# Optimization experiments

Hardware: AMD Instinct MI355X
Metric: run time of the kernel (lower is better)

The kernel has to match this reference:

```python
import jax, jax.numpy as jnp
import numpy as np

H = 2048; HQ = 16; HKV = 4; G = HQ // HKV; D = 128; S = 2048
KS = 32; KSTRIDE = 16; BS = 128; TOPK = 8
INIT_BLK = 1; LOCAL_BLK = 2; WIN = 512
THETA = 500000.0
N_CMP = (S - KS) // KSTRIDE + 1
N_BLK = S // BS
NEG = -1e30


def _rope_inv_freq():
    # llama3-style frequency scaling (factor 8, high 4, low 1, orig 8192)
    inv = 1.0 / (THETA ** (np.arange(0, D, 2, dtype=np.float64) / D))
    factor, lo_f, hi_f, orig = 8.0, 1.0, 4.0, 8192.0
    wav = 2.0 * np.pi / inv
    smooth = (orig / wav - lo_f) / (hi_f - lo_f)
    inv_s = np.where(wav > orig / lo_f, inv / factor,
                     np.where(wav < orig / hi_f, inv,
                              (1.0 - smooth) * inv / factor + smooth * inv))
    return jnp.asarray(inv_s, dtype=jnp.float32)


def _rope(x):
    # x: [S, h, D]
    ang = jnp.arange(x.shape[0], dtype=jnp.float32)[:, None] * _rope_inv_freq()[None, :]
    cos = jnp.cos(ang)[:, None, :]
    sin = jnp.sin(ang)[:, None, :]
    x1, x2 = x[..., : D // 2], x[..., D // 2:]
    return jnp.concatenate([x1 * cos - x2 * sin, x2 * cos + x1 * sin], axis=-1)


def setup_inputs() -> dict:
    key = jax.random.key(0)
    ks = jax.random.split(key, 8)
    std = 0.02
    return {
        'hidden_states': jax.random.normal(ks[0], (1, S, H), jnp.float32),
        'Wq': jax.random.normal(ks[1], (H, HQ * D), jnp.float32) * std,
        'Wk': jax.random.normal(ks[2], (H, HKV * D), jnp.float32) * std,
        'Wv': jax.random.normal(ks[3], (H, HKV * D), jnp.float32) * std,
        'Wo': jax.random.normal(ks[4], (HQ * D, H), jnp.float32) * std,
        'Wg': jax.random.normal(ks[5], (H, HQ * 3), jnp.float32) * std,
        'Wck': jax.random.normal(ks[6], (HKV, KS * D, D), jnp.float32) * std,
        'Wcv': jax.random.normal(ks[7], (HKV, KS * D, D), jnp.float32) * std,
    }


def _nsa_forward(hidden_states, Wq, Wk, Wv, Wo, Wg, Wck, Wcv):
    x = hidden_states[0]                                  # [S, H] (bsz=1, packed)
    q = _rope((x @ Wq).reshape(S, HQ, D))                 # [S, HQ, D]
    k = _rope((x @ Wk).reshape(S, HKV, D))                # [S, HKV, D]
    v = (x @ Wv).reshape(S, HKV, D)
    scale = D ** -0.5
    pos = jnp.arange(S)
    qg = q.reshape(S, HKV, G, D)

    # ---- branch 1: compressed attention (overlapping windows, learned pooling) ----
    starts = jnp.arange(N_CMP) * KSTRIDE
    widx = starts[:, None] + jnp.arange(KS)[None, :]      # [N_CMP, KS]
    kw = k[widx].transpose(2, 0, 1, 3).reshape(HKV, N_CMP, KS * D)
    vw = v[widx].transpose(2, 0, 1, 3).reshape(HKV, N_CMP, KS * D)
    ck = jnp.einsum('hnf,hfd->hnd', kw, Wck)              # [HKV, N_CMP, D]
    cv = jnp.einsum('hnf,hfd->hnd', vw, Wcv)
    s_cmp = jnp.einsum('shgd,hnd->hgsn', qg, ck) * scale  # [HKV, G, S, N_CMP]
    m_cmp = (starts + KS)[None, :] <= pos[:, None] + 1    # fully-past compressed blocks
    has_cmp = m_cmp.any(axis=-1).astype(s_cmp.dtype)      # [S]
    p_cmp = jax.nn.softmax(jnp.where(m_cmp[None, None], s_cmp, NEG), axis=-1)
    p_cmp = p_cmp * has_cmp[None, None, :, None]
    o_cmp = jnp.einsum('hgsn,hnd->shgd', p_cmp, cv).reshape(S, HQ, D)

    # ---- branch 2: top-k block-selected attention ----
    cmp2blk = (starts // BS)[:, None] == jnp.arange(N_BLK)[None, :]
    bscore = jnp.einsum('hgsn,nb->hsb', p_cmp, cmp2blk.astype(p_cmp.dtype))  # GQA-group sum
    qblk = pos // BS
    blks = jnp.arange(N_BLK)
    forced = (blks[None, :] < INIT_BLK) | ((blks[None, :] <= qblk[:, None]) & (blks[None, :] > qblk[:, None] - LOCAL_BLK))
    _, top_idx = jax.lax.top_k(bscore + forced[None].astype(bscore.dtype) * 1e9, TOPK)
    sel_blk = jnp.any(top_idx[..., None] == blks, axis=-2)  # [HKV, S, N_BLK]

    causal = pos[None, :] <= pos[:, None]                    # [S, S]
    raw = jnp.einsum('shgd,nhd->hgsn', qg, k) * scale        # [HKV, G, S, S] (shared by branches 2/3)

    m_sel = jnp.repeat(sel_blk, BS, axis=-1) & causal[None]  # [HKV, S, S]
    p_sel = jax.nn.softmax(jnp.where(m_sel[:, None], raw, NEG), axis=-1)
    o_sel = jnp.einsum('hgsn,nhd->shgd', p_sel, v).reshape(S, HQ, D)

    # ---- branch 3: sliding-window attention ----
    m_win = causal & (pos[None, :] > pos[:, None] - WIN)
    p_win = jax.nn.softmax(jnp.where(m_win[None, None], raw, NEG), axis=-1)
    o_win = jnp.einsum('hgsn,nhd->shgd', p_win, v).reshape(S, HQ, D)

    # ---- per-head sigmoid gates mixing the three branches ----
    g = jax.nn.sigmoid(x @ Wg).reshape(S, HQ, 3)
    o = g[..., 0:1] * o_cmp + g[..., 1:2] * o_sel + g[..., 2:3] * o_win
    return (o.reshape(S, HQ * D) @ Wo)[None]                 # [1, S, H]


def reference(hidden_states, Wq, Wk, Wv, Wo, Wg, Wck, Wcv):
    return _nsa_forward(hidden_states, Wq, Wk, Wv, Wo, Wg, Wck, Wcv)
```

## Files before the change

### kernel.cpp

```cpp
#include <hip/hip_runtime.h>
#include <math.h>

#define SS 2048
#define HH 2048
#define HQ 16
#define HKV 4
#define GG 4
#define DD 128
#define KS 32
#define KSTRIDE 16
#define NCMP 127
#define NBLK 16
#define TOPK 8
#define WINSZ 512
#define TQ 16

typedef unsigned short u16;
typedef __bf16 bf16x8 __attribute__((ext_vector_type(8)));
typedef __bf16 bf16x4 __attribute__((ext_vector_type(4)));
typedef float f32x4 __attribute__((ext_vector_type(4)));

__device__ __forceinline__ u16 f2bf(float f) {
    __bf16 b = (__bf16)f;
    return __builtin_bit_cast(u16, b);
// ... 189 lines not shown
            bf16x8 af[4], bf[4];
#pragma unroll
            for (int mi = 0; mi < 4; ++mi) {
                int row = wm * 64 + mi * 16 + lr;
                int g = (kk * 4 + hi) ^ (row & 7);
                af[mi] = *reinterpret_cast<const bf16x8*>(&Asm[row * 64 + g * 8]);
            }
#pragma unroll
            for (int ni = 0; ni < 4; ++ni) {
                int row = wn * 64 + ni * 16 + lr;
                int g = (kk * 4 + hi) ^ (row & 7);
                bf[ni] = *reinterpret_cast<const bf16x8*>(&Bsm[row * 64 + g * 8]);
            }
#pragma unroll
            for (int mi = 0; mi < 4; ++mi)
#pragma unroll
                for (int ni = 0; ni < 4; ++ni)
                    acc[mi][ni] = __builtin_amdgcn_mfma_f32_16x16x32_bf16(af[mi], bf[ni], acc[mi][ni], 0, 0, 0);
        }
    }
#pragma unroll
    for (int mi = 0; mi < 4; ++mi) {
#pragma unroll
        for (int ni = 0; ni < 4; ++ni) {
            int col = bn + wn * 64 + ni * 16 + lr;
            if (col < N) {
#pragma unroll
                for (int r = 0; r < 4; ++r) {
                    int row = bm + wm * 64 + mi * 16 + hi * 4 + r;
                    C[(size_t)row * N + col] = acc[mi][ni][r];
                }
            }
        }
    }
}

__global__ __launch_bounds__(256) void cmp_kv_split(const u16* __restrict__ Ak,
                                                    const u16* __restrict__ Wkt,
                                                    const u16* __restrict__ Av,
                                                    const u16* __restrict__ Wvt,
                                                    float* __restrict__ partials) {
    __shared__ __align__(16) u16 Asm[128 * 64];
    __shared__ __align__(16) u16 Bsm[128 * 64];
    int z = blockIdx.y, split = blockIdx.x;
    int h = z & 3;
    const u16* A  = (z >> 2) ? Av : Ak;
    const u16* Wt = (z >> 2) ? Wvt : Wkt;
    int t = threadIdx.x, lane = t & 63, w = t >> 6;
    int wm = w >> 1, wn = w & 1;
    int lr = lane & 15, hi = lane >> 4;
    const u16* Wh = Wt + (size_t)h * DD * (KS * DD);

    f32x4 acc[4][4] = {};
    int kbase = split * 512;
    for (int it = 0; it < 8; ++it) {
        int k0 = kbase + it * 64;
        if (it) __syncthreads();
        int roff = k0 >> 7;
        int dbase = ((k0 >> 6) & 1) * 64;
#pragma unroll
        for (int i = 0; i < 4; ++i) {
            int cflat = i * 256 + t;
            int m = cflat >> 3;
            int g = cflat & 7;
            int gl = g ^ (m & 7);
            unsigned lofs = (unsigned)((i * 256 + (t & ~63)) * 16);
            int nr = (m < NCMP) ? m : (NCMP - 1);
            gload16(A + ((size_t)(nr * KSTRIDE + roff) * HKV + h) * DD + dbase + gl * 8,
                    (char*)Asm + lofs);
            gload16(Wh + (size_t)m * (KS * DD) + k0 + gl * 8, (char*)Bsm + lofs);
        }
        __syncthreads();
#pragma unroll
        for (int kk = 0; kk < 2; ++kk) {
            bf16x8 af[4], bf[4];
#pragma unroll
            for (int mi = 0; mi < 4; ++mi) {
                int row = wm * 64 + mi * 16 + lr;
                int g = (kk * 4 + hi) ^ (row & 7);
                af[mi] = *reinterpret_cast<const bf16x8*>(&Asm[row * 64 + g * 8]);
            }
#pragma unroll
            for (int ni = 0; ni < 4; ++ni) {
                int row = wn * 64 + ni * 16 + lr;
                int g = (kk * 4 + hi) ^ (row & 7);
                bf[ni] = *reinterpret_cast<const bf16x8*>(&Bsm[row * 64 + g * 8]);
            }
#pragma unroll
            for (int mi = 0; mi < 4; ++mi)
#pragma unroll
                for (int ni = 0; ni < 4; ++ni)
                    acc[mi][ni] = __builtin_amdgcn_mfma_f32_16x16x32_bf16(af[mi], bf[ni], acc[mi][ni], 0, 0, 0);
        }
    }
    float* Cout = partials + ((size_t)(z * 8 + split)) * 128 * 128;
#pragma unroll
    for (int mi = 0; mi < 4; ++mi)
#pragma unroll
        for (int ni = 0; ni < 4; ++ni) {
            int col = wn * 64 + ni * 16 + lr;
#pragma unroll
            for (int r = 0; r < 4; ++r) {
                int row = wm * 64 + mi * 16 + hi * 4 + r;
                Cout[(size_t)row * 128 + col] = acc[mi][ni][r];
            }
        }
}

__global__ void cmp_kv_reduce(const float* __restrict__ partials,
                              u16* __restrict__ ckbf, u16* __restrict__ cvtbf) {
    int row = blockIdx.x, z = blockIdx.y, col = threadIdx.x;
    float s = 0.f;
#pragma unroll
    for (int sp = 0; sp < 8; ++sp)
        s += partials[(((size_t)z * 8 + sp) * 128 + row) * 128 + col];
    if (z < 4) ckbf[((size_t)z * 128 + row) * 128 + col] = f2bf(s);
    else       cvtbf[((size_t)(z - 4) * 128 + col) * 128 + row] = f2bf(s);
}

__global__ __launch_bounds__(256) void cmp_attn_mfma(
    const u16* __restrict__ qbf,
    const u16* __restrict__ ckbf,
    const u16* __restrict__ cvtbf,
    const float* __restrict__ gate,
    float* __restrict__ o_acc,
    unsigned int* __restrict__ sel) {
    __shared__ __align__(16) u16 Cks[128 * 128];
    __shared__ __align__(16) u16 P2[4][16 * 128];
    __shared__ float bs[4][16][16];
    int t = threadIdx.x, lane = t & 63, w = t >> 6;
    int lr = lane & 15, hi = lane >> 4;
    int s0 = blockIdx.x * 16, h = blockIdx.y;
    int hq = h * GG + w;
    int sr = s0 + lr;
    const u16* ckh = ckbf + (size_t)h * 128 * 128;
    const u16* cvh = cvtbf + (size_t)h * 128 * 128;
    bf16x8 qf[4];
#pragma unroll
    for (int ks = 0; ks < 4; ++ks)
        qf[ks] = *reinterpret_cast<const bf16x8*>(
            &qbf[((size_t)sr * HQ + hq) * DD + ks * 32 + hi * 8]);
#pragma unroll
    for (int i = 0; i < 8; ++i) {
        int id = i * 256 + t;
        int key = id >> 4, sub = id & 15;
        gload16(ckh + (size_t)key * 128 + ((sub ^ (key & 7)) * 8),
                (char*)Cks + (id & ~63) * 16);
    }
    __syncthreads();
    f32x4 sacc[8] = {};
#pragma unroll
    for (int ks = 0; ks < 4; ++ks)
#pragma unroll
        for (int mt = 0; mt < 8; ++mt) {
            int row = mt * 16 + lr;
            bf16x8 kf = *reinterpret_cast<const bf16x8*>(
                &Cks[row * 128 + (((ks * 4 + hi) ^ (row & 7)) * 8)]);
            sacc[mt] = __builtin_amdgcn_mfma_f32_16x16x32_bf16(kf, qf[ks], sacc[mt], 0, 0, 0);
        }
    int nv = (sr >= 31) ? ((sr - 31) >> 4) + 1 : 0;
    float e[8][4];
    float mx = -1e30f;
#pragma unroll
    for (int mt = 0; mt < 8; ++mt)
#pragma unroll
        for (int r = 0; r < 4; ++r) {
            int n = mt * 16 + hi * 4 + r;
            float x = (n < nv) ? sacc[mt][r] : -1e30f;
            e[mt][r] = x;
            mx = fmaxf(mx, x);
        }
    mx = fmaxf(mx, __shfl_xor(mx, 16, 64));
    mx = fmaxf(mx, __shfl_xor(mx, 32, 64));
    float l = 0.f;
#pragma unroll
    for (int mt = 0; mt < 8; ++mt)
#pragma unroll
        for (int r = 0; r < 4; ++r) {
            int n = mt * 16 + hi * 4 + r;
            float p = (n < nv) ? __expf(e[mt][r] - mx) : 0.f;
            e[mt][r] = p;
            l += p;
        }
    l += __shfl_xor(l, 16, 64);
    l += __shfl_xor(l, 32, 64);
    float invl = (nv > 0) ? 1.f / l : 0.f;
#pragma unroll
    for (int mt = 0; mt < 8; ++mt)
#pragma unroll
        for (int r = 0; r < 4; ++r) e[mt][r] *= invl;
#pragma unroll
    for (int mt = 0; mt < 8; ++mt) {
        bf16x4 pk;
        pk[0] = (__bf16)e[mt][0]; pk[1] = (__bf16)e[mt][1];
        pk[2] = (__bf16)e[mt][2]; pk[3] = (__bf16)e[mt][3];
        int grp = mt * 2 + (hi >> 1);
        int idx = lr * 128 + ((grp ^ (lr & 7)) * 8) + (hi & 1) * 4;
        *reinterpret_cast<bf16x4*>(&P2[w][idx]) = pk;
    }
#pragma unroll
    for (int mt = 0; mt < 8; ++mt) {
        float s4 = e[mt][0] + e[mt][1] + e[mt][2] + e[mt][3];
        float v = s4 + __shfl_xor(s4, 16, 64);
        if (hi == 0) bs[w][lr][mt * 2] = v;
        else if (hi == 2) bs[w][lr][mt * 2 + 1] = v;
    }
    __syncthreads();
    bf16x8 pa[4];
#pragma unroll
    for (int kslot = 0; kslot < 4; ++kslot)
        pa[kslot] = *reinterpret_cast<const bf16x8*>(
            &P2[w][lr * 128 + (((kslot * 4 + hi) ^ (lr & 7)) * 8)]);
    f32x4 Os[8] = {};
#pragma unroll
    for (int nt = 0; nt < 8; ++nt) {
        int d = nt * 16 + lr;
#pragma unroll
        for (int kslot = 0; kslot < 4; ++kslot) {
            bf16x8 bv = *reinterpret_cast<const bf16x8*>(
                &cvh[(size_t)d * 128 + kslot * 32 + hi * 8]);
            Os[nt] = __builtin_amdgcn_mfma_f32_16x16x32_bf16(pa[kslot], bv, Os[nt], 0, 0, 0);
        }
    }
#pragma unroll
    for (int r = 0; r < 4; ++r) {
        int q = hi * 4 + r;
        int srow = s0 + q;
        float g0 = gate[((size_t)srow * HQ + hq) * 3 + 0];
#pragma unroll
        for (int nt = 0; nt < 8; ++nt) {
            size_t idx = ((size_t)srow * HQ + hq) * DD + nt * 16 + lr;
            o_acc[idx] = g0 * Os[nt][r];
        }
    }
    if (t < 16) {
        int q = t, s = s0 + q;
        int qblk = s >> 7;
#pragma unroll
        for (int b = 0; b < 16; ++b) {
            bool forced = (b == 0) || (b <= qblk && b > qblk - 2);
            bs[0][q][b] = bs[0][q][b] + bs[1][q][b] + bs[2][q][b] + bs[3][q][b]
                          + (forced ? 1e9f : 0.f);
        }
        unsigned int mask = 0;
        for (int it = 0; it < TOPK; ++it) {
            int arg = 0; float best = bs[0][q][0];
            for (int b = 1; b < 16; ++b) {
                float x = bs[0][q][b];
                if (x > best) { best = x; arg = b; }
            }
            mask |= 1u << arg;
            bs[0][q][arg] = -1e38f;
        }
        sel[s * HKV + h] = mask;
    }
}

__global__ __launch_bounds__(256, 3) void sel_win_mfma(
    const u16* __restrict__ qbf,
    const u16* __restrict__ kbf,
    const u16* __restrict__ vtbf,
    const float* __restrict__ gate,
    const unsigned int* __restrict__ sel,
    float* __restrict__ o_acc) {
    __shared__ __align__(16) u16 Ks[64 * 128];
    __shared__ __align__(16) u16 Vs[128 * 64];
    __shared__ __align__(16) u16 P2[4][2][16 * 64];
    __shared__ unsigned int sml[16];
    int t = threadIdx.x, lane = t & 63, w = t >> 6;
    int lr = lane & 15, hi = lane >> 4;
    int s0 = (gridDim.x - 1 - blockIdx.x) * 16;
    int h = blockIdx.y;
    int hq = h * GG + w;
    int sr = s0 + lr;
    if (t < 16) sml[t] = sel[(s0 + t) * HKV + h];
    bf16x8 qf[4];
#pragma unroll
    for (int ks = 0; ks < 4; ++ks)
        qf[ks] = *reinterpret_cast<const bf16x8*>(
            &qbf[((size_t)(s0 + lr) * HQ + hq) * DD + ks * 32 + hi * 8]);
    __syncthreads();
    unsigned mymask = sml[lr];
    unsigned orMask = 0;
#pragma unroll
    for (int i = 0; i < 16; ++i) orMask |= sml[i];
    float m_u = -1e30f, l_s = 0.f, l_w = 0.f;
    f32x4 Os[8] = {}, Ow[8] = {};
    int smax = s0 + 15;
    const u16* vbase = vtbf + (size_t)h * DD * SS;

    for (int kb = 0; kb * 128 <= smax; ++kb) {
        bool needSel = (orMask >> kb) & 1u;
        bool selbit = needSel && ((mymask >> kb) & 1u);
        for (int half = 0; half < 2; ++half) {
            int hst = kb * 128 + half * 64;
            if (hst > smax) break;
            bool hWin = (hst + 63 >= s0 - (WINSZ - 1));
            if (!(needSel || hWin)) continue;
            __syncthreads();
#pragma unroll
            for (int i = 0; i < 4; ++i) {
                int id = i * 256 + t;
                int key = id >> 4, dq = id & 15;
                gload16(kbf + ((size_t)(hst + key) * HKV + h) * DD + ((dq ^ (key & 7)) * 8),
                        (char*)Ks + (id & ~63) * 16);
                int d = id >> 3, kq = id & 7;
                gload16(vbase + (size_t)d * SS + hst + ((kq ^ (d & 7)) * 8),
                        (char*)Vs + (id & ~63) * 16);
            }
            __syncthreads();
            f32x4 sacc[4] = {};
#pragma unroll
            for (int ks = 0; ks < 4; ++ks) {
#pragma unroll
                for (int mt = 0; mt < 4; ++mt) {
                    int key = mt * 16 + lr;
                    bf16x8 kf = *reinterpret_cast<const bf16x8*>(
                        &Ks[key * 128 + (((ks * 4 + hi) ^ (key & 7)) * 8)]);
                    sacc[mt] = __builtin_amdgcn_mfma_f32_16x16x32_bf16(kf, qf[ks], sacc[mt], 0, 0, 0);
                }
            }
            float e4[4][4];
            float mx = -1e30f;
#pragma unroll
            for (int mt = 0; mt < 4; ++mt)
#pragma unroll
                for (int r = 0; r < 4; ++r) {
                    int key = hst + mt * 16 + hi * 4 + r;
                    bool vS = selbit && (key <= sr);
                    bool vW = hWin && (key <= sr) && (key > sr - WINSZ);
                    float e = (vS || vW) ? sacc[mt][r] : -1e30f;
                    e4[mt][r] = e;
                    mx = fmaxf(mx, e);
                }
            mx = fmaxf(mx, __shfl_xor(mx, 16, 64));
            mx = fmaxf(mx, __shfl_xor(mx, 32, 64));
            if (!__all(mx - m_u <= 8.f)) {
                float newm = fmaxf(m_u, mx);
                float corr = __expf(m_u - newm);
                m_u = newm;
                l_s *= corr; l_w *= corr;
#pragma unroll
                for (int r = 0; r < 4; ++r) {
                    float c2 = __shfl(corr, hi * 4 + r, 64);
#pragma unroll
                    for (int nt = 0; nt < 8; ++nt) { Os[nt][r] *= c2; Ow[nt][r] *= c2; }
                }
            }
            float lsA = 0.f, lwA = 0.f;
#pragma unroll
            for (int mt = 0; mt < 4; ++mt)
#pragma unroll
                for (int r = 0; r < 4; ++r) {
                    int key = hst + mt * 16 + hi * 4 + r;
                    bool vS = selbit && (key <= sr);
                    bool vW = hWin && (key <= sr) && (key > sr - WINSZ);
                    float e = (vS || vW) ? __expf(e4[mt][r] - m_u) : 0.f;
                    e4[mt][r] = e;
                    lsA += vS ? e : 0.f;
                    lwA += vW ? e : 0.f;
                }
            lsA += __shfl_xor(lsA, 16, 64); lsA += __shfl_xor(lsA, 32, 64);
            lwA += __shfl_xor(lwA, 16, 64); lwA += __shfl_xor(lwA, 32, 64);
            l_s += lsA; l_w += lwA;
            if (needSel) {
#pragma unroll
                for (int mt = 0; mt < 4; ++mt) {
                    bf16x4 pk;
#pragma unroll
                    for (int r = 0; r < 4; ++r) {
                        int key = hst + mt * 16 + hi * 4 + r;
                        bool vS = selbit && (key <= sr);
                        pk[r] = (__bf16)(vS ? e4[mt][r] : 0.f);
                    }
                    int grp = mt * 2 + (hi >> 1);
                    int idx = lr * 64 + ((grp ^ (lr & 7)) * 8) + (hi & 1) * 4;
                    *reinterpret_cast<bf16x4*>(&P2[w][0][idx]) = pk;
                }
            }
            if (hWin) {
#pragma unroll
                for (int mt = 0; mt < 4; ++mt) {
                    bf16x4 pk;
#pragma unroll
                    for (int r = 0; r < 4; ++r) {
                        int key = hst + mt * 16 + hi * 4 + r;
                        bool vW = (key <= sr) && (key > sr - WINSZ);
                        pk[r] = (__bf16)(vW ? e4[mt][r] : 0.f);
                    }
                    int grp = mt * 2 + (hi >> 1);
                    int idx = lr * 64 + ((grp ^ (lr & 7)) * 8) + (hi & 1) * 4;
                    *reinterpret_cast<bf16x4*>(&P2[w][1][idx]) = pk;
                }
            }
            bf16x8 pas0, pas1, paw0, paw1;
            if (needSel) {
                pas0 = *reinterpret_cast<const bf16x8*>(&P2[w][0][lr * 64 + (((0 + hi) ^ (lr & 7)) * 8)]);
                pas1 = *reinterpret_cast<const bf16x8*>(&P2[w][0][lr * 64 + (((4 + hi) ^ (lr & 7)) * 8)]);
            }
            if (hWin) {
                paw0 = *reinterpret_cast<const bf16x8*>(&P2[w][1][lr * 64 + (((0 + hi) ^ (lr & 7)) * 8)]);
                paw1 = *reinterpret_cast<const bf16x8*>(&P2[w][1][lr * 64 + (((4 + hi) ^ (lr & 7)) * 8)]);
            }
#pragma unroll
            for (int nt = 0; nt < 8; ++nt) {
                int d = nt * 16 + lr;
                bf16x8 bv0 = *reinterpret_cast<const bf16x8*>(&Vs[d * 64 + (((0 + hi) ^ (d & 7)) * 8)]);
                bf16x8 bv1 = *reinterpret_cast<const bf16x8*>(&Vs[d * 64 + (((4 + hi) ^ (d & 7)) * 8)]);
                if (needSel) {
                    Os[nt] = __builtin_amdgcn_mfma_f32_16x16x32_bf16(pas0, bv0, Os[nt], 0, 0, 0);
                    Os[nt] = __builtin_amdgcn_mfma_f32_16x16x32_bf16(pas1, bv1, Os[nt], 0, 0, 0);
                }
                if (hWin) {
                    Ow[nt] = __builtin_amdgcn_mfma_f32_16x16x32_bf16(paw0, bv0, Ow[nt], 0, 0, 0);
                    Ow[nt] = __builtin_amdgcn_mfma_f32_16x16x32_bf16(paw1, bv1, Ow[nt], 0, 0, 0);
                }
            }
        }
    }
    float invls = (l_s > 0.f) ? 1.f / l_s : 0.f;
    float invlw = (l_w > 0.f) ? 1.f / l_w : 0.f;
#pragma unroll
    for (int r = 0; r < 4; ++r) {
        int q = hi * 4 + r;
        int srow = s0 + q;
        float a1 = gate[((size_t)srow * HQ + hq) * 3 + 1] * __shfl(invls, q, 64);
        float a2 = gate[((size_t)srow * HQ + hq) * 3 + 2] * __shfl(invlw, q, 64);
#pragma unroll
        for (int nt = 0; nt < 8; ++nt) {
            size_t idx = ((size_t)srow * HQ + hq) * DD + nt * 16 + lr;
            o_acc[idx] += a1 * Os[nt][r] + a2 * Ow[nt][r];
        }
    }
}

extern "C" void kernel_launch(void* const* d_in, const int* in_sizes, int n_in,
                              void* d_out, int out_size, void* d_ws, size_t ws_size,
                              hipStream_t stream) {
    const float* x   = (const float*)d_in[0];
    const float* Wq  = (const float*)d_in[1];
    const float* Wk  = (const float*)d_in[2];
    const float* Wv  = (const float*)d_in[3];
    const float* Wo  = (const float*)d_in[4];
    const float* Wg  = (const float*)d_in[5];
    const float* Wck = (const float*)d_in[6];
    const float* Wcv = (const float*)d_in[7];
    float* out = (float*)d_out;
    char* w = (char*)d_ws;
    float* qb   = (float*)(w + 0);
    float* kb   = (float*)(w + 16777216);
    float* vb   = (float*)(w + 20971520);
    float* g3   = (float*)(w + 25165824);
    u16* ckbf   = (u16*)(w + 25559040);
    u16* cvtbf  = (u16*)(w + 25819136);
    unsigned int* selb = (unsigned int*)(w + 26079232);
    float* cost = (float*)(w + 26112000);
    float* sint = (float*)(w + 26636288);
    float* oacc = (float*)(w + 27160576);
    u16* xb     = (u16*)(w + 43937792);
    u16* oaccb  = (u16*)(w + 52326400);
    u16* Wq_t   = (u16*)(w + 60715008);
    u16* Wo_t   = (u16*)(w + 69103616);
    u16* Wk_t   = (u16*)(w + 77492224);
    u16* Wv_t   = (u16*)(w + 79589376);
    u16* Wg_t   = (u16*)(w + 81686528);
    u16* qbf = Wq_t;
    u16* kbf = Wk_t;
    u16* vtbf = Wv_t;
    u16* vbf = (u16*)kb;
    u16* Wck_t = oaccb;
    u16* Wcv_t = xb;
    float* partials = oacc;

    hipLaunchKernelGGL(rope_tab, dim3(SS), dim3(64), 0, stream, cost, sint);
    hipLaunchKernelGGL(conv_bf16, dim3(4096), dim3(256), 0, stream, x, xb, SS * HH / 4);
    hipLaunchKernelGGL(convT, dim3(64, 64), dim3(256), 0, stream, Wq, Wq_t, HH, 2048, 2048, 0, 0);
    hipLaunchKernelGGL(convT, dim3(64, 16), dim3(256), 0, stream, Wk, Wk_t, HH, 512, 512, 0, 0);
    hipLaunchKernelGGL(convT, dim3(64, 16), dim3(256), 0, stream, Wv, Wv_t, HH, 512, 512, 0, 0);
    hipLaunchKernelGGL(convT, dim3(64, 4),  dim3(256), 0, stream, Wg, Wg_t, HH, 48, 128, 0, 0);
    hipLaunchKernelGGL(convT, dim3(64, 64), dim3(256), 0, stream, Wo, Wo_t, HQ * DD, 2048, 2048, 0, 0);
    hipLaunchKernelGGL(gemm_proj, dim3(25, 16), dim3(256), 0, stream,
                       xb, Wq_t, Wk_t, Wv_t, Wg_t, qb, kb, vb, g3);
    hipLaunchKernelGGL(rope_bf16, dim3(SS, HQ),  dim3(64), 0, stream, qb, qbf, cost, sint, HQ, 0.08838834764831845f);
    hipLaunchKernelGGL(rope_bf16, dim3(SS, HKV), dim3(64), 0, stream, kb, kbf, cost, sint, HKV, 1.0f);
    hipLaunchKernelGGL(sigmoid_k, dim3((SS * HQ * 3 + 255) / 256), dim3(256), 0, stream, g3, SS * HQ * 3);
    hipLaunchKernelGGL(conv_bf16, dim3(1024), dim3(256), 0, stream, vb, vbf, SS * HKV * DD / 4);
    hipLaunchKernelGGL(conv_vt, dim3(64, 4, 4), dim3(256), 0, stream, vb, vtbf);
    hipLaunchKernelGGL(convT, dim3(128, 4, 4), dim3(256), 0, stream,
                       Wck, Wck_t, KS * DD, DD, DD, (size_t)KS * DD * DD, (size_t)DD * KS * DD);
    hipLaunchKernelGGL(convT, dim3(128, 4, 4), dim3(256), 0, stream,
                       Wcv, Wcv_t, KS * DD, DD, DD, (size_t)KS * DD * DD, (size_t)DD * KS * DD);
    hipLaunchKernelGGL(cmp_kv_split, dim3(8, 8), dim3(256), 0, stream,
                       kbf, Wck_t, vbf, Wcv_t, partials);
    hipLaunchKernelGGL(cmp_kv_reduce, dim3(128, 8), dim3(128), 0, stream,
                       partials, ckbf, cvtbf);
    hipLaunchKernelGGL(cmp_attn_mfma, dim3(SS / TQ, HKV), dim3(256), 0, stream,
                       qbf, ckbf, cvtbf, g3, oacc, selb);
    hipLaunchKernelGGL(sel_win_mfma, dim3(SS / TQ, HKV), dim3(256), 0, stream,
                       qbf, kbf, vtbf, g3, selb, oacc);
    hipLaunchKernelGGL(conv_bf16, dim3(4096), dim3(256), 0, stream, oacc, oaccb, SS * HQ * DD / 4);
    hipLaunchKernelGGL(gemm_mfma, dim3(16, 16), dim3(256), 0, stream, oaccb, Wo_t, out, 2048, 2048, 2048);
}
```

Measured before the change: 266.1 us.

## Fuse compressed and selected/window attention into one kernel; widen cmp-KV split

Merges the compressed-attention kernel and the selection/sliding-window kernel into a single attn_fused kernel. The top-k block mask now passes through shared memory, and the final output is written directly as bf16, which removes the fp32 o_acc round trip, the separate sel buffer and the conv_bf16 launch. Shared memory is reused between the compressed KV tile and the K/V tiles. The cmp_kv_split grid is also doubled to 16 splits with half the K range each, giving more parallelism at the cost of a larger reduction. The fused kernel holds the extra Oc accumulators in registers, which may raise register pressure under launch bounds of 3.

```diff
diff --git a/kernel.cpp b/kernel.cpp
--- a/kernel.cpp
+++ b/kernel.cpp
@@ -265,8 +265,8 @@
     const u16* Wh = Wt + (size_t)h * DD * (KS * DD);
 
     f32x4 acc[4][4] = {};
-    int kbase = split * 512;
-    for (int it = 0; it < 8; ++it) {
+    int kbase = split * 256;
+    for (int it = 0; it < 4; ++it) {
         int k0 = kbase + it * 64;
         if (it) __syncthreads();
         int roff = k0 >> 7;
@@ -306,7 +306,7 @@
                     acc[mi][ni] = __builtin_amdgcn_mfma_f32_16x16x32_bf16(af[mi], bf[ni], acc[mi][ni], 0, 0, 0);
         }
     }
-    float* Cout = partials + ((size_t)(z * 8 + split)) * 128 * 128;
+    float* Cout = partials + ((size_t)(z * 16 + split)) * 128 * 128;
 #pragma unroll
     for (int mi = 0; mi < 4; ++mi)
 #pragma unroll
@@ -325,160 +325,23 @@
     int row = blockIdx.x, z = blockIdx.y, col = threadIdx.x;
     float s = 0.f;
 #pragma unroll
-    for (int sp = 0; sp < 8; ++sp)
-        s += partials[(((size_t)z * 8 + sp) * 128 + row) * 128 + col];
+    for (int sp = 0; sp < 16; ++sp)
+        s += partials[(((size_t)z * 16 + sp) * 128 + row) * 128 + col];
     if (z < 4) ckbf[((size_t)z * 128 + row) * 128 + col] = f2bf(s);
     else       cvtbf[((size_t)(z - 4) * 128 + col) * 128 + row] = f2bf(s);
 }
 
-__global__ __launch_bounds__(256) void cmp_attn_mfma(
+__global__ __launch_bounds__(256, 3) void attn_fused(
     const u16* __restrict__ qbf,
+    const u16* __restrict__ kbf,
+    const u16* __restrict__ vtbf,
     const u16* __restrict__ ckbf,
     const u16* __restrict__ cvtbf,
     const float* __restrict__ gate,
-    float* __restrict__ o_acc,
-    unsigned int* __restrict__ sel) {
-    __shared__ __align__(16) u16 Cks[128 * 128];
-    __shared__ __align__(16) u16 P2[4][16 * 128];
+    u16* __restrict__ outb) {
+    __shared__ __align__(16) u16 KV[128 * 128];
+    __shared__ __align__(16) u16 P2s[4][2048];
     __shared__ float bs[4][16][16];
-    int t = threadIdx.x, lane = t & 63, w = t >> 6;
-    int lr = lane & 15, hi = lane >> 4;
-    int s0 = blockIdx.x * 16, h = blockIdx.y;
-    int hq = h * GG + w;
-    int sr = s0 + lr;
-    const u16* ckh = ckbf + (size_t)h * 128 * 128;
-    const u16* cvh = cvtbf + (size_t)h * 128 * 128;
-    bf16x8 qf[4];
-#pragma unroll
-    for (int ks = 0; ks < 4; ++ks)
-        qf[ks] = *reinterpret_cast<const bf16x8*>(
-            &qbf[((size_t)sr * HQ + hq) * DD + ks * 32 + hi * 8]);
-#pragma unroll
-    for (int i = 0; i < 8; ++i) {
-        int id = i * 256 + t;
-        int key = id >> 4, sub = id & 15;
-        gload16(ckh + (size_t)key * 128 + ((sub ^ (key & 7)) * 8),
-                (char*)Cks + (id & ~63) * 16);
-    }
-    __syncthreads();
-    f32x4 sacc[8] = {};
-#pragma unroll
-    for (int ks = 0; ks < 4; ++ks)
-#pragma unroll
-        for (int mt = 0; mt < 8; ++mt) {
-            int row = mt * 16 + lr;
-            bf16x8 kf = *reinterpret_cast<const bf16x8*>(
-                &Cks[row * 128 + (((ks * 4 + hi) ^ (row & 7)) * 8)]);
-            sacc[mt] = __builtin_amdgcn_mfma_f32_16x16x32_bf16(kf, qf[ks], sacc[mt], 0, 0, 0);
-        }
-    int nv = (sr >= 31) ? ((sr - 31) >> 4) + 1 : 0;
-    float e[8][4];
-    float mx = -1e30f;
-#pragma unroll
-    for (int mt = 0; mt < 8; ++mt)
-#pragma unroll
-        for (int r = 0; r < 4; ++r) {
-            int n = mt * 16 + hi * 4 + r;
-            float x = (n < nv) ? sacc[mt][r] : -1e30f;
-            e[mt][r] = x;
-            mx = fmaxf(mx, x);
-        }
-    mx = fmaxf(mx, __shfl_xor(mx, 16, 64));
-    mx = fmaxf(mx, __shfl_xor(mx, 32, 64));
-    float l = 0.f;
-#pragma unroll
-    for (int mt = 0; mt < 8; ++mt)
-#pragma unroll
-        for (int r = 0; r < 4; ++r) {
-            int n = mt * 16 + hi * 4 + r;
-            float p = (n < nv) ? __expf(e[mt][r] - mx) : 0.f;
-            e[mt][r] = p;
-            l += p;
-        }
-    l += __shfl_xor(l, 16, 64);
-    l += __shfl_xor(l, 32, 64);
-    float invl = (nv > 0) ? 1.f / l : 0.f;
-#pragma unroll
-    for (int mt = 0; mt < 8; ++mt)
-#pragma unroll
-        for (int r = 0; r < 4; ++r) e[mt][r] *= invl;
-#pragma unroll
-    for (int mt = 0; mt < 8; ++mt) {
-        bf16x4 pk;
-        pk[0] = (__bf16)e[mt][0]; pk[1] = (__bf16)e[mt][1];
-        pk[2] = (__bf16)e[mt][2]; pk[3] = (__bf16)e[mt][3];
-        int grp = mt * 2 + (hi >> 1);
-        int idx = lr * 128 + ((grp ^ (lr & 7)) * 8) + (hi & 1) * 4;
-        *reinterpret_cast<bf16x4*>(&P2[w][idx]) = pk;
-    }
-#pragma unroll
-    for (int mt = 0; mt < 8; ++mt) {
-        float s4 = e[mt][0] + e[mt][1] + e[mt][2] + e[mt][3];
-        float v = s4 + __shfl_xor(s4, 16, 64);
-        if (hi == 0) bs[w][lr][mt * 2] = v;
-        else if (hi == 2) bs[w][lr][mt * 2 + 1] = v;
-    }
-    __syncthreads();
-    bf16x8 pa[4];
-#pragma unroll
-    for (int kslot = 0; kslot < 4; ++kslot)
-        pa[kslot] = *reinterpret_cast<const bf16x8*>(
-            &P2[w][lr * 128 + (((kslot * 4 + hi) ^ (lr & 7)) * 8)]);
-    f32x4 Os[8] = {};
-#pragma unroll
-    for (int nt = 0; nt < 8; ++nt) {
-        int d = nt * 16 + lr;
-#pragma unroll
-        for (int kslot = 0; kslot < 4; ++kslot) {
-            bf16x8 bv = *reinterpret_cast<const bf16x8*>(
-                &cvh[(size_t)d * 128 + kslot * 32 + hi * 8]);
-            Os[nt] = __builtin_amdgcn_mfma_f32_16x16x32_bf16(pa[kslot], bv, Os[nt], 0, 0, 0);
-        }
-    }
-#pragma unroll
-    for (int r = 0; r < 4; ++r) {
-        int q = hi * 4 + r;
-        int srow = s0 + q;
-        float g0 = gate[((size_t)srow * HQ + hq) * 3 + 0];
-#pragma unroll
-        for (int nt = 0; nt < 8; ++nt) {
-            size_t idx = ((size_t)srow * HQ + hq) * DD + nt * 16 + lr;
-            o_acc[idx] = g0 * Os[nt][r];
-        }
-    }
-    if (t < 16) {
-        int q = t, s = s0 + q;
-        int qblk = s >> 7;
-#pragma unroll
-        for (int b = 0; b < 16; ++b) {
-            bool forced = (b == 0) || (b <= qblk && b > qblk - 2);
-            bs[0][q][b] = bs[0][q][b] + bs[1][q][b] + bs[2][q][b] + bs[3][q][b]
-                          + (forced ? 1e9f : 0.f);
-        }
-        unsigned int mask = 0;
-        for (int it = 0; it < TOPK; ++it) {
-            int arg = 0; float best = bs[0][q][0];
-            for (int b = 1; b < 16; ++b) {
-                float x = bs[0][q][b];
-                if (x > best) { best = x; arg = b; }
-            }
-            mask |= 1u << arg;
-            bs[0][q][arg] = -1e38f;
-        }
-        sel[s * HKV + h] = mask;
-    }
-}
-
-__global__ __launch_bounds__(256, 3) void sel_win_mfma(
-    const u16* __restrict__ qbf,
-    const u16* __restrict__ kbf,
-    const u16* __restrict__ vtbf,
-    const float* __restrict__ gate,
-    const unsigned int* __restrict__ sel,
-    float* __restrict__ o_acc) {
-    __shared__ __align__(16) u16 Ks[64 * 128];
-    __shared__ __align__(16) u16 Vs[128 * 64];
-    __shared__ __align__(16) u16 P2[4][2][16 * 64];
     __shared__ unsigned int sml[16];
     int t = threadIdx.x, lane = t & 63, w = t >> 6;
     int lr = lane & 15, hi = lane >> 4;
@@ -486,13 +349,131 @@
     int h = blockIdx.y;
     int hq = h * GG + w;
     int sr = s0 + lr;
-    if (t < 16) sml[t] = sel[(s0 + t) * HKV + h];
+    const u16* ckh = ckbf + (size_t)h * 128 * 128;
+    const u16* cvh = cvtbf + (size_t)h * 128 * 128;
     bf16x8 qf[4];
 #pragma unroll
     for (int ks = 0; ks < 4; ++ks)
         qf[ks] = *reinterpret_cast<const bf16x8*>(
-            &qbf[((size_t)(s0 + lr) * HQ + hq) * DD + ks * 32 + hi * 8]);
+            &qbf[((size_t)sr * HQ + hq) * DD + ks * 32 + hi * 8]);
+
+#pragma unroll
+    for (int i = 0; i < 8; ++i) {
+        int id = i * 256 + t;
+        int key = id >> 4, sub = id & 15;
+        gload16(ckh + (size_t)key * 128 + ((sub ^ (key & 7)) * 8),
+                (char*)KV + (id & ~63) * 16);
+    }
     __syncthreads();
+    f32x4 sacc8[8] = {};
+#pragma unroll
+    for (int ks = 0; ks < 4; ++ks)
+#pragma unroll
+        for (int mt = 0; mt < 8; ++mt) {
+            int row = mt * 16 + lr;
+            bf16x8 kf = *reinterpret_cast<const bf16x8*>(
+                &KV[row * 128 + (((ks * 4 + hi) ^ (row & 7)) * 8)]);
+            sacc8[mt] = __builtin_amdgcn_mfma_f32_16x16x32_bf16(kf, qf[ks], sacc8[mt], 0, 0, 0);
+        }
+    int nv = (sr >= 31) ? ((sr - 31) >> 4) + 1 : 0;
+    {
+        float e[8][4];
+        float mx = -1e30f;
+#pragma unroll
+        for (int mt = 0; mt < 8; ++mt)
+#pragma unroll
+            for (int r = 0; r < 4; ++r) {
+                int n = mt * 16 + hi * 4 + r;
+                float x = (n < nv) ? sacc8[mt][r] : -1e30f;
+                e[mt][r] = x;
+                mx = fmaxf(mx, x);
+            }
+        mx = fmaxf(mx, __shfl_xor(mx, 16, 64));
+        mx = fmaxf(mx, __shfl_xor(mx, 32, 64));
+        float l = 0.f;
+#pragma unroll
+        for (int mt = 0; mt < 8; ++mt)
+#pragma unroll
+            for (int r = 0; r < 4; ++r) {
+                int n = mt * 16 + hi * 4 + r;
+                float p = (n < nv) ? __expf(e[mt][r] - mx) : 0.f;
+                e[mt][r] = p;
+                l += p;
+            }
+        l += __shfl_xor(l, 16, 64);
+        l += __shfl_xor(l, 32, 64);
+        float invl = (nv > 0) ? 1.f / l : 0.f;
+#pragma unroll
+        for (int mt = 0; mt < 8; ++mt)
+#pragma unroll
+            for (int r = 0; r < 4; ++r) e[mt][r] *= invl;
+#pragma unroll
+        for (int mt = 0; mt < 8; ++mt) {
+            bf16x4 pk;
+            pk[0] = (__bf16)e[mt][0]; pk[1] = (__bf16)e[mt][1];
+            pk[2] = (__bf16)e[mt][2]; pk[3] = (__bf16)e[mt][3];
+            int grp = mt * 2 + (hi >> 1);
+            int idx = lr * 128 + ((grp ^ (lr & 7)) * 8) + (hi & 1) * 4;
+            *reinterpret_cast<bf16x4*>(&P2s[w][idx]) = pk;
+        }
+#pragma unroll
+        for (int mt = 0; mt < 8; ++mt) {
+            float s4 = e[mt][0] + e[mt][1] + e[mt][2] + e[mt][3];
+            float v = s4 + __shfl_xor(s4, 16, 64);
+            if (hi == 0) bs[w][lr][mt * 2] = v;
+            else if (hi == 2) bs[w][lr][mt * 2 + 1] = v;
+        }
+    }
+    __syncthreads();
+    f32x4 Oc[8] = {};
+    {
+        bf16x8 pa[4];
+#pragma unroll
+        for (int kslot = 0; kslot < 4; ++kslot)
+            pa[kslot] = *reinterpret_cast<const bf16x8*>(
+                &P2s[w][lr * 128 + (((kslot * 4 + hi) ^ (lr & 7)) * 8)]);
+#pragma unroll
+        for (int nt = 0; nt < 8; ++nt) {
+            int d = nt * 16 + lr;
+#pragma unroll
+            for (int kslot = 0; kslot < 4; ++kslot) {
+                bf16x8 bv = *reinterpret_cast<const bf16x8*>(
+                    &cvh[(size_t)d * 128 + kslot * 32 + hi * 8]);
+                Oc[nt] = __builtin_amdgcn_mfma_f32_16x16x32_bf16(pa[kslot], bv, Oc[nt], 0, 0, 0);
+            }
+        }
+    }
+#pragma unroll
+    for (int r = 0; r < 4; ++r) {
+        float g0 = gate[((size_t)(s0 + hi * 4 + r) * HQ + hq) * 3 + 0];
+#pragma unroll
+        for (int nt = 0; nt < 8; ++nt) Oc[nt][r] *= g0;
+    }
+    if (t < 16) {
+        int q = t, s = s0 + q;
+        int qblk = s >> 7;
+#pragma unroll
+        for (int b = 0; b < 16; ++b) {
+            bool forced = (b == 0) || (b <= qblk && b > qblk - 2);
+            bs[0][q][b] = bs[0][q][b] + bs[1][q][b] + bs[2][q][b] + bs[3][q][b]
+                          + (forced ? 1e9f : 0.f);
+        }
+        unsigned int mask = 0;
+        for (int it = 0; it < TOPK; ++it) {
+            int arg = 0; float best = bs[0][q][0];
+            for (int b = 1; b < 16; ++b) {
+                float x = bs[0][q][b];
+                if (x > best) { best = x; arg = b; }
+            }
+            mask |= 1u << arg;
+            bs[0][q][arg] = -1e38f;
+        }
+        sml[q] = mask;
+    }
+    __syncthreads();
+
+    u16* Ks = KV;
+    u16* Vs = KV + 64 * 128;
     unsigned mymask = sml[lr];
     unsigned orMask = 0;
 #pragma unroll
@@ -588,7 +569,7 @@
                     }
                     int grp = mt * 2 + (hi >> 1);
                     int idx = lr * 64 + ((grp ^ (lr & 7)) * 8) + (hi & 1) * 4;
-                    *reinterpret_cast<bf16x4*>(&P2[w][0][idx]) = pk;
+                    *reinterpret_cast<bf16x4*>(&P2s[w][idx]) = pk;
                 }
             }
             if (hWin) {
@@ -602,18 +583,18 @@
                         pk[r] = (__bf16)(vW ? e4[mt][r] : 0.f);
                     }
                     int grp = mt * 2 + (hi >> 1);
-                    int idx = lr * 64 + ((grp ^ (lr & 7)) * 8) + (hi & 1) * 4;
-                    *reinterpret_cast<bf16x4*>(&P2[w][1][idx]) = pk;
+                    int idx = 1024 + lr * 64 + ((grp ^ (lr & 7)) * 8) + (hi & 1) * 4;
+                    *reinterpret_cast<bf16x4*>(&P2s[w][idx]) = pk;
                 }
             }
             bf16x8 pas0, pas1, paw0, paw1;
             if (needSel) {
-                pas0 = *reinterpret_cast<const bf16x8*>(&P2[w][0][lr * 64 + (((0 + hi) ^ (lr & 7)) * 8)]);
-                pas1 = *reinterpret_cast<const bf16x8*>(&P2[w][0][lr * 64 + (((4 + hi) ^ (lr & 7)) * 8)]);
+                pas0 = *reinterpret_cast<const bf16x8*>(&P2s[w][lr * 64 + (((0 + hi) ^ (lr & 7)) * 8)]);
+                pas1 = *reinterpret_cast<const bf16x8*>(&P2s[w][lr * 64 + (((4 + hi) ^ (lr & 7)) * 8)]);
             }
             if (hWin) {
-                paw0 = *reinterpret_cast<const bf16x8*>(&P2[w][1][lr * 64 + (((0 + hi) ^ (lr & 7)) * 8)]);
-                paw1 = *reinterpret_cast<const bf16x8*>(&P2[w][1][lr * 64 + (((4 + hi) ^ (lr & 7)) * 8)]);
+                paw0 = *reinterpret_cast<const bf16x8*>(&P2s[w][1024 + lr * 64 + (((0 + hi) ^ (lr & 7)) * 8)]);
+                paw1 = *reinterpret_cast<const bf16x8*>(&P2s[w][1024 + lr * 64 + (((4 + hi) ^ (lr & 7)) * 8)]);
             }
 #pragma unroll
             for (int nt = 0; nt < 8; ++nt) {
@@ -642,7 +623,7 @@
 #pragma unroll
         for (int nt = 0; nt < 8; ++nt) {
             size_t idx = ((size_t)srow * HQ + hq) * DD + nt * 16 + lr;
-            o_acc[idx] += a1 * Os[nt][r] + a2 * Ow[nt][r];
+            outb[idx] = f2bf(Oc[nt][r] + a1 * Os[nt][r] + a2 * Ow[nt][r]);
         }
     }
 }
@@ -666,7 +647,6 @@
     float* g3   = (float*)(w + 25165824);
     u16* ckbf   = (u16*)(w + 25559040);
     u16* cvtbf  = (u16*)(w + 25819136);
-    unsigned int* selb = (unsigned int*)(w + 26079232);
     float* cost = (float*)(w + 26112000);
     float* sint = (float*)(w + 26636288);
     float* oacc = (float*)(w + 27160576);
@@ -703,14 +683,11 @@
                        Wck, Wck_t, KS * DD, DD, DD, (size_t)KS * DD * DD, (size_t)DD * KS * DD);
     hipLaunchKernelGGL(convT, dim3(128, 4, 4), dim3(256), 0, stream,
                        Wcv, Wcv_t, KS * DD, DD, DD, (size_t)KS * DD * DD, (size_t)DD * KS * DD);
-    hipLaunchKernelGGL(cmp_kv_split, dim3(8, 8), dim3(256), 0, stream,
+    hipLaunchKernelGGL(cmp_kv_split, dim3(16, 8), dim3(256), 0, stream,
                        kbf, Wck_t, vbf, Wcv_t, partials);
     hipLaunchKernelGGL(cmp_kv_reduce, dim3(128, 8), dim3(128), 0, stream,
                        partials, ckbf, cvtbf);
-    hipLaunchKernelGGL(cmp_attn_mfma, dim3(SS / TQ, HKV), dim3(256), 0, stream,
-                       qbf, ckbf, cvtbf, g3, oacc, selb);
-    hipLaunchKernelGGL(sel_win_mfma, dim3(SS / TQ, HKV), dim3(256), 0, stream,
-                       qbf, kbf, vtbf, g3, selb, oacc);
-    hipLaunchKernelGGL(conv_bf16, dim3(4096), dim3(256), 0, stream, oacc, oaccb, SS * HQ * DD / 4);
+    hipLaunchKernelGGL(attn_fused, dim3(SS / TQ, HKV), dim3(256), 0, stream,
+                       qbf, kbf, vtbf, ckbf, cvtbf, g3, oaccb);
     hipLaunchKernelGGL(gemm_mfma, dim3(16, 16), dim3(256), 0, stream, oaccb, Wo_t, out, 2048, 2048, 2048);
 }
```

New measurement: 316.5 us. +18.9%, slower.

## Share K/V tiles across two query groups in sel_win and fuse bf16 output conversion

Applied to the files above, without the earlier changes.

The selection/window attention kernel now uses 512-thread blocks covering 32 query rows. Each K/V tile loaded to LDS therefore serves two 16-row groups, halving redundant tile loads and the number of blocks. It also writes the final bf16 output directly, removing the separate conversion kernel, and adds s_setprio around the MFMA sections. The compressed KV split-K GEMM is split 16 ways instead of 8 for more parallelism, at the cost of more partial-sum traffic. Both 16-row groups in a block now iterate over the union of needed tiles, with idle groups waiting at barriers.

```diff
diff --git a/kernel.cpp b/kernel.cpp
--- a/kernel.cpp
+++ b/kernel.cpp
@@ -265,8 +265,8 @@
     const u16* Wh = Wt + (size_t)h * DD * (KS * DD);
 
     f32x4 acc[4][4] = {};
-    int kbase = split * 512;
-    for (int it = 0; it < 8; ++it) {
+    int kbase = split * 256;
+    for (int it = 0; it < 4; ++it) {
         int k0 = kbase + it * 64;
         if (it) __syncthreads();
         int roff = k0 >> 7;
@@ -306,7 +306,7 @@
                     acc[mi][ni] = __builtin_amdgcn_mfma_f32_16x16x32_bf16(af[mi], bf[ni], acc[mi][ni], 0, 0, 0);
         }
     }
-    float* Cout = partials + ((size_t)(z * 8 + split)) * 128 * 128;
+    float* Cout = partials + ((size_t)(z * 16 + split)) * 128 * 128;
 #pragma unroll
     for (int mi = 0; mi < 4; ++mi)
 #pragma unroll
@@ -325,8 +325,8 @@
     int row = blockIdx.x, z = blockIdx.y, col = threadIdx.x;
     float s = 0.f;
 #pragma unroll
-    for (int sp = 0; sp < 8; ++sp)
-        s += partials[(((size_t)z * 8 + sp) * 128 + row) * 128 + col];
+    for (int sp = 0; sp < 16; ++sp)
+        s += partials[(((size_t)z * 16 + sp) * 128 + row) * 128 + col];
     if (z < 4) ckbf[((size_t)z * 128 + row) * 128 + col] = f2bf(s);
     else       cvtbf[((size_t)(z - 4) * 128 + col) * 128 + row] = f2bf(s);
 }
@@ -469,51 +469,55 @@
     }
 }
 
-__global__ __launch_bounds__(256, 3) void sel_win_mfma(
+__global__ __launch_bounds__(512, 4) void sel_win_mfma(
     const u16* __restrict__ qbf,
     const u16* __restrict__ kbf,
     const u16* __restrict__ vtbf,
     const float* __restrict__ gate,
     const unsigned int* __restrict__ sel,
-    float* __restrict__ o_acc) {
+    const float* __restrict__ oacc,
+    u16* __restrict__ outb) {
     __shared__ __align__(16) u16 Ks[64 * 128];
     __shared__ __align__(16) u16 Vs[128 * 64];
-    __shared__ __align__(16) u16 P2[4][2][16 * 64];
-    __shared__ unsigned int sml[16];
+    __shared__ __align__(16) u16 P2s[8][2048];
+    __shared__ unsigned int sml[32];
     int t = threadIdx.x, lane = t & 63, w = t >> 6;
     int lr = lane & 15, hi = lane >> 4;
-    int s0 = (gridDim.x - 1 - blockIdx.x) * 16;
+    int s0b = (gridDim.x - 1 - blockIdx.x) * 32;
     int h = blockIdx.y;
-    int hq = h * GG + w;
+    int rg = w >> 2;
+    int hq = h * GG + (w & 3);
+    int s0 = s0b + rg * 16;
     int sr = s0 + lr;
-    if (t < 16) sml[t] = sel[(s0 + t) * HKV + h];
+    if (t < 32) sml[t] = sel[(s0b + t) * HKV + h];
     bf16x8 qf[4];
 #pragma unroll
     for (int ks = 0; ks < 4; ++ks)
         qf[ks] = *reinterpret_cast<const bf16x8*>(
-            &qbf[((size_t)(s0 + lr) * HQ + hq) * DD + ks * 32 + hi * 8]);
+            &qbf[((size_t)sr * HQ + hq) * DD + ks * 32 + hi * 8]);
     __syncthreads();
-    unsigned mymask = sml[lr];
-    unsigned orMask = 0;
-#pragma unroll
-    for (int i = 0; i < 16; ++i) orMask |= sml[i];
+    unsigned mymask = sml[rg * 16 + lr];
+    unsigned orW = 0, orB = 0;
+#pragma unroll
+    for (int i = 0; i < 16; ++i) orW |= sml[rg * 16 + i];
+#pragma unroll
+    for (int i = 0; i < 32; ++i) orB |= sml[i];
     float m_u = -1e30f, l_s = 0.f, l_w = 0.f;
     f32x4 Os[8] = {}, Ow[8] = {};
-    int smax = s0 + 15;
+    int smaxB = s0b + 31;
     const u16* vbase = vtbf + (size_t)h * DD * SS;
 
-    for (int kb = 0; kb * 128 <= smax; ++kb) {
-        bool needSel = (orMask >> kb) & 1u;
-        bool selbit = needSel && ((mymask >> kb) & 1u);
+    for (int kb = 0; kb * 128 <= smaxB; ++kb) {
+        bool needSelB = (orB >> kb) & 1u;
         for (int half = 0; half < 2; ++half) {
             int hst = kb * 128 + half * 64;
-            if (hst > smax) break;
-            bool hWin = (hst + 63 >= s0 - (WINSZ - 1));
-            if (!(needSel || hWin)) continue;
+            if (hst > smaxB) break;
+            bool hWinB = (hst + 63 >= s0b - (WINSZ - 1));
+            if (!(needSelB || hWinB)) continue;
             __syncthreads();
 #pragma unroll
-            for (int i = 0; i < 4; ++i) {
-                int id = i * 256 + t;
+            for (int i = 0; i < 2; ++i) {
+                int id = i * 512 + t;
                 int key = id >> 4, dq = id & 15;
                 gload16(kbf + ((size_t)(hst + key) * HKV + h) * DD + ((dq ^ (key & 7)) * 8),
                         (char*)Ks + (id & ~63) * 16);
@@ -522,112 +526,122 @@
                         (char*)Vs + (id & ~63) * 16);
             }
             __syncthreads();
-            f32x4 sacc[4] = {};
-#pragma unroll
-            for (int ks = 0; ks < 4; ++ks) {
-#pragma unroll
-                for (int mt = 0; mt < 4; ++mt) {
-                    int key = mt * 16 + lr;
-                    bf16x8 kf = *reinterpret_cast<const bf16x8*>(
-                        &Ks[key * 128 + (((ks * 4 + hi) ^ (key & 7)) * 8)]);
-                    sacc[mt] = __builtin_amdgcn_mfma_f32_16x16x32_bf16(kf, qf[ks], sacc[mt], 0, 0, 0);
-                }
-            }
-            float e4[4][4];
-            float mx = -1e30f;
-#pragma unroll
-            for (int mt = 0; mt < 4; ++mt)
-#pragma unroll
-                for (int r = 0; r < 4; ++r) {
-                    int key = hst + mt * 16 + hi * 4 + r;
-                    bool vS = selbit && (key <= sr);
-                    bool vW = hWin && (key <= sr) && (key > sr - WINSZ);
-                    float e = (vS || vW) ? sacc[mt][r] : -1e30f;
-                    e4[mt][r] = e;
-                    mx = fmaxf(mx, e);
-                }
-            mx = fmaxf(mx, __shfl_xor(mx, 16, 64));
-            mx = fmaxf(mx, __shfl_xor(mx, 32, 64));
-            if (!__all(mx - m_u <= 8.f)) {
-                float newm = fmaxf(m_u, mx);
-                float corr = __expf(m_u - newm);
-                m_u = newm;
-                l_s *= corr; l_w *= corr;
-#pragma unroll
-                for (int r = 0; r < 4; ++r) {
-                    float c2 = __shfl(corr, hi * 4 + r, 64);
-#pragma unroll
-                    for (int nt = 0; nt < 8; ++nt) { Os[nt][r] *= c2; Ow[nt][r] *= c2; }
-                }
-            }
-            float lsA = 0.f, lwA = 0.f;
-#pragma unroll
-            for (int mt = 0; mt < 4; ++mt)
-#pragma unroll
-                for (int r = 0; r < 4; ++r) {
-                    int key = hst + mt * 16 + hi * 4 + r;
-                    bool vS = selbit && (key <= sr);
-                    bool vW = hWin && (key <= sr) && (key > sr - WINSZ);
-                    float e = (vS || vW) ? __expf(e4[mt][r] - m_u) : 0.f;
-                    e4[mt][r] = e;
-                    lsA += vS ? e : 0.f;
-                    lwA += vW ? e : 0.f;
-                }
-            lsA += __shfl_xor(lsA, 16, 64); lsA += __shfl_xor(lsA, 32, 64);
-            lwA += __shfl_xor(lwA, 16, 64); lwA += __shfl_xor(lwA, 32, 64);
-            l_s += lsA; l_w += lwA;
-            if (needSel) {
-#pragma unroll
-                for (int mt = 0; mt < 4; ++mt) {
-                    bf16x4 pk;
+            bool act = (hst <= s0 + 15);
+            bool needSel = act && ((orW >> kb) & 1u);
+            bool selbit = needSel && ((mymask >> kb) & 1u);
+            bool hWin = act && (hst + 63 >= s0 - (WINSZ - 1));
+            if (needSel || hWin) {
+                f32x4 sacc[4] = {};
+                __builtin_amdgcn_s_setprio(1);
+#pragma unroll
+                for (int ks = 0; ks < 4; ++ks) {
+#pragma unroll
+                    for (int mt = 0; mt < 4; ++mt) {
+                        int key = mt * 16 + lr;
+                        bf16x8 kf = *reinterpret_cast<const bf16x8*>(
+                            &Ks[key * 128 + (((ks * 4 + hi) ^ (key & 7)) * 8)]);
+                        sacc[mt] = __builtin_amdgcn_mfma_f32_16x16x32_bf16(kf, qf[ks], sacc[mt], 0, 0, 0);
+                    }
+                }
+                __builtin_amdgcn_s_setprio(0);
+                float e4[4][4];
+                float mx = -1e30f;
+#pragma unroll
+                for (int mt = 0; mt < 4; ++mt)
 #pragma unroll
                     for (int r = 0; r < 4; ++r) {
                         int key = hst + mt * 16 + hi * 4 + r;
                         bool vS = selbit && (key <= sr);
-                        pk[r] = (__bf16)(vS ? e4[mt][r] : 0.f);
+                        bool vW = hWin && (key <= sr) && (key > sr - WINSZ);
+                        float e = (vS || vW) ? sacc[mt][r] : -1e30f;
+                        e4[mt][r] = e;
+                        mx = fmaxf(mx, e);
                     }
-                    int grp = mt * 2 + (hi >> 1);
-                    int idx = lr * 64 + ((grp ^ (lr & 7)) * 8) + (hi & 1) * 4;
-                    *reinterpret_cast<bf16x4*>(&P2[w][0][idx]) = pk;
-                }
-            }
-            if (hWin) {
-#pragma unroll
-                for (int mt = 0; mt < 4; ++mt) {
-                    bf16x4 pk;
+                mx = fmaxf(mx, __shfl_xor(mx, 16, 64));
+                mx = fmaxf(mx, __shfl_xor(mx, 32, 64));
+                if (!__all(mx - m_u <= 8.f)) {
+                    float newm = fmaxf(m_u, mx);
+                    float corr = __expf(m_u - newm);
+                    m_u = newm;
+                    l_s *= corr; l_w *= corr;
+#pragma unroll
+                    for (int r = 0; r < 4; ++r) {
+                        float c2 = __shfl(corr, hi * 4 + r, 64);
+#pragma unroll
+                        for (int nt = 0; nt < 8; ++nt) { Os[nt][r] *= c2; Ow[nt][r] *= c2; }
+                    }
+                }
+                float lsA = 0.f, lwA = 0.f;
+#pragma unroll
+                for (int mt = 0; mt < 4; ++mt)
 #pragma unroll
                     for (int r = 0; r < 4; ++r) {
                         int key = hst + mt * 16 + hi * 4 + r;
-                        bool vW = (key <= sr) && (key > sr - WINSZ);
-                        pk[r] = (__bf16)(vW ? e4[mt][r] : 0.f);
+                        bool vS = selbit && (key <= sr);
+                        bool vW = hWin && (key <= sr) && (key > sr - WINSZ);
+                        float e = (vS || vW) ? __expf(e4[mt][r] - m_u) : 0.f;
+                        e4[mt][r] = e;
+                        lsA += vS ? e : 0.f;
+                        lwA += vW ? e : 0.f;
                     }
-                    int grp = mt * 2 + (hi >> 1);
-                    int idx = lr * 64 + ((grp ^ (lr & 7)) * 8) + (hi & 1) * 4;
-                    *reinterpret_cast<bf16x4*>(&P2[w][1][idx]) = pk;
-                }
-            }
-            bf16x8 pas0, pas1, paw0, paw1;
-            if (needSel) {
-                pas0 = *reinterpret_cast<const bf16x8*>(&P2[w][0][lr * 64 + (((0 + hi) ^ (lr & 7)) * 8)]);
-                pas1 = *reinterpret_cast<const bf16x8*>(&P2[w][0][lr * 64 + (((4 + hi) ^ (lr & 7)) * 8)]);
-            }
-            if (hWin) {
-                paw0 = *reinterpret_cast<const bf16x8*>(&P2[w][1][lr * 64 + (((0 + hi) ^ (lr & 7)) * 8)]);
-                paw1 = *reinterpret_cast<const bf16x8*>(&P2[w][1][lr * 64 + (((4 + hi) ^ (lr & 7)) * 8)]);
-            }
-#pragma unroll
-            for (int nt = 0; nt < 8; ++nt) {
-                int d = nt * 16 + lr;
-                bf16x8 bv0 = *reinterpret_cast<const bf16x8*>(&Vs[d * 64 + (((0 + hi) ^ (d & 7)) * 8)]);
-                bf16x8 bv1 = *reinterpret_cast<const bf16x8*>(&Vs[d * 64 + (((4 + hi) ^ (d & 7)) * 8)]);
+                lsA += __shfl_xor(lsA, 16, 64); lsA += __shfl_xor(lsA, 32, 64);
+                lwA += __shfl_xor(lwA, 16, 64); lwA += __shfl_xor(lwA, 32, 64);
+                l_s += lsA; l_w += lwA;
                 if (needSel) {
-                    Os[nt] = __builtin_amdgcn_mfma_f32_16x16x32_bf16(pas0, bv0, Os[nt], 0, 0, 0);
-                    Os[nt] = __builtin_amdgcn_mfma_f32_16x16x32_bf16(pas1, bv1, Os[nt], 0, 0, 0);
+#pragma unroll
+                    for (int mt = 0; mt < 4; ++mt) {
+                        bf16x4 pk;
+#pragma unroll
+                        for (int r = 0; r < 4; ++r) {
+                            int key = hst + mt * 16 + hi * 4 + r;
+                            bool vS = selbit && (key <= sr);
+                            pk[r] = (__bf16)(vS ? e4[mt][r] : 0.f);
+                        }
+                        int grp = mt * 2 + (hi >> 1);
+                        int idx = lr * 64 + ((grp ^ (lr & 7)) * 8) + (hi & 1) * 4;
+                        *reinterpret_cast<bf16x4*>(&P2s[w][idx]) = pk;
+                    }
                 }
                 if (hWin) {
-                    Ow[nt] = __builtin_amdgcn_mfma_f32_16x16x32_bf16(paw0, bv0, Ow[nt], 0, 0, 0);
-                    Ow[nt] = __builtin_amdgcn_mfma_f32_16x16x32_bf16(paw1, bv1, Ow[nt], 0, 0, 0);
-                }
+#pragma unroll
+                    for (int mt = 0; mt < 4; ++mt) {
+                        bf16x4 pk;
+#pragma unroll
+                        for (int r = 0; r < 4; ++r) {
+                            int key = hst + mt * 16 + hi * 4 + r;
+                            bool vW = (key <= sr) && (key > sr - WINSZ);
+                            pk[r] = (__bf16)(vW ? e4[mt][r] : 0.f);
+                        }
+                        int grp = mt * 2 + (hi >> 1);
+                        int idx = 1024 + lr * 64 + ((grp ^ (lr & 7)) * 8) + (hi & 1) * 4;
+                        *reinterpret_cast<bf16x4*>(&P2s[w][idx]) = pk;
+                    }
+                }
+                bf16x8 pas0, pas1, paw0, paw1;
+                if (needSel) {
+                    pas0 = *reinterpret_cast<const bf16x8*>(&P2s[w][lr * 64 + (((0 + hi) ^ (lr & 7)) * 8)]);
+                    pas1 = *reinterpret_cast<const bf16x8*>(&P2s[w][lr * 64 + (((4 + hi) ^ (lr & 7)) * 8)]);
+                }
+                if (hWin) {
+                    paw0 = *reinterpret_cast<const bf16x8*>(&P2s[w][1024 + lr * 64 + (((0 + hi) ^ (lr & 7)) * 8)]);
+                    paw1 = *reinterpret_cast<const bf16x8*>(&P2s[w][1024 + lr * 64 + (((4 + hi) ^ (lr & 7)) * 8)]);
+                }
+                __builtin_amdgcn_s_setprio(1);
+#pragma unroll
+                for (int nt = 0; nt < 8; ++nt) {
+                    int d = nt * 16 + lr;
+                    bf16x8 bv0 = *reinterpret_cast<const bf16x8*>(&Vs[d * 64 + (((0 + hi) ^ (d & 7)) * 8)]);
+                    bf16x8 bv1 = *reinterpret_cast<const bf16x8*>(&Vs[d * 64 + (((4 + hi) ^ (d & 7)) * 8)]);
+                    if (needSel) {
+                        Os[nt] = __builtin_amdgcn_mfma_f32_16x16x32_bf16(pas0, bv0, Os[nt], 0, 0, 0);
+                        Os[nt] = __builtin_amdgcn_mfma_f32_16x16x32_bf16(pas1, bv1, Os[nt], 0, 0, 0);
+                    }
+                    if (hWin) {
+                        Ow[nt] = __builtin_amdgcn_mfma_f32_16x16x32_bf16(paw0, bv0, Ow[nt], 0, 0, 0);
+                        Ow[nt] = __builtin_amdgcn_mfma_f32_16x16x32_bf16(paw1, bv1, Ow[nt], 0, 0, 0);
+                    }
+                }
+                __builtin_amdgcn_s_setprio(0);
             }
         }
     }
@@ -642,7 +656,7 @@
 #pragma unroll
         for (int nt = 0; nt < 8; ++nt) {
             size_t idx = ((size_t)srow * HQ + hq) * DD + nt * 16 + lr;
-            o_acc[idx] += a1 * Os[nt][r] + a2 * Ow[nt][r];
+            outb[idx] = f2bf(oacc[idx] + a1 * Os[nt][r] + a2 * Ow[nt][r]);
         }
     }
 }
@@ -703,14 +717,13 @@
                        Wck, Wck_t, KS * DD, DD, DD, (size_t)KS * DD * DD, (size_t)DD * KS * DD);
     hipLaunchKernelGGL(convT, dim3(128, 4, 4), dim3(256), 0, stream,
                        Wcv, Wcv_t, KS * DD, DD, DD, (size_t)KS * DD * DD, (size_t)DD * KS * DD);
-    hipLaunchKernelGGL(cmp_kv_split, dim3(8, 8), dim3(256), 0, stream,
+    hipLaunchKernelGGL(cmp_kv_split, dim3(16, 8), dim3(256), 0, stream,
                        kbf, Wck_t, vbf, Wcv_t, partials);
     hipLaunchKernelGGL(cmp_kv_reduce, dim3(128, 8), dim3(128), 0, stream,
                        partials, ckbf, cvtbf);
     hipLaunchKernelGGL(cmp_attn_mfma, dim3(SS / TQ, HKV), dim3(256), 0, stream,
                        qbf, ckbf, cvtbf, g3, oacc, selb);
-    hipLaunchKernelGGL(sel_win_mfma, dim3(SS / TQ, HKV), dim3(256), 0, stream,
-                       qbf, kbf, vtbf, g3, selb, oacc);
-    hipLaunchKernelGGL(conv_bf16, dim3(4096), dim3(256), 0, stream, oacc, oaccb, SS * HQ * DD / 4);
+    hipLaunchKernelGGL(sel_win_mfma, dim3(SS / 32, HKV), dim3(512), 0, stream,
+                       qbf, kbf, vtbf, g3, selb, oacc, oaccb);
     hipLaunchKernelGGL(gemm_mfma, dim3(16, 16), dim3(256), 0, stream, oaccb, Wo_t, out, 2048, 2048, 2048);
 }
```

Result: slower. 348.6 us (+31.0%).
